# Kernel tuning notes

Measured on AMD Instinct MI355X. Metric: run time of the kernel, lower is better.

## Reference

```python
import jax, jax.numpy as jnp
import numpy as np

N, IN, H, C = 50000, 128, 4, 32
E = 800000
NEG_SLOPE = 0.2


def setup_inputs() -> dict:
    key = jax.random.key(0)
    ks = jax.random.split(key, 8)
    x = jax.random.normal(ks[0], (N, IN), dtype=jnp.float32)
    edge_index = jax.random.randint(ks[1], (2, E), 0, N, dtype=jnp.int64)
    s = 0.1
    W = jax.random.normal(ks[2], (H * C, IN), dtype=jnp.float32) * s
    att_src = jax.random.normal(ks[3], (1, H, C), dtype=jnp.float32) * s
    att_dst = jax.random.normal(ks[4], (1, H, C), dtype=jnp.float32) * s
    bias = jnp.zeros((H * C,), dtype=jnp.float32)
    skip_W = jax.random.normal(ks[5], (H * C, IN), dtype=jnp.float32) * s
    skip_b = jnp.zeros((H * C,), dtype=jnp.float32)
    return {"x": x, "edge_index": edge_index, "W": W, "att_src": att_src,
            "att_dst": att_dst, "bias": bias, "skip_W": skip_W, "skip_b": skip_b}


def reference(x, edge_index, W, att_src, att_dst, bias, skip_W, skip_b):
    src, dst = edge_index[0], edge_index[1]
    # projected node features: [N, H, C]
    xp = (x @ W.T).reshape(N, H, C)
    # per-node attention logits: [N, H]
    a_src = jnp.sum(xp * att_src, axis=-1)
    a_dst = jnp.sum(xp * att_dst, axis=-1)
    # edge logits with LeakyReLU: [E, H]
    e = a_src[src] + a_dst[dst]
    e = jnp.where(e > 0, e, NEG_SLOPE * e)
    # segment softmax over incoming edges of each dst node
    m = jax.ops.segment_max(e, dst, num_segments=N)  # [N, H]
    ex = jnp.exp(e - m[dst])
    denom = jax.ops.segment_sum(ex, dst, num_segments=N)  # [N, H]
    alpha = ex / (denom[dst] + 1e-16)
    # weighted messages and scatter-add aggregation: [N, H, C]
    msg = alpha[:, :, None] * xp[src]
    agg = jax.ops.segment_sum(msg, dst, num_segments=N)
    x_gat = agg.reshape(N, H * C) + bias
    x_skip = x @ skip_W.T + skip_b
    return jax.nn.elu(x_gat + x_skip)
```

## Files before the change

kernel.cpp:

```cpp
#include <hip/hip_runtime.h>
#include <hip/hip_bf16.h>


#define NN 50000
#define EE 800000
#define FD 128
#define NEG_SLOPE 0.2f

#define ROWU 136
#define SCB 1024
#define NB_SC ((NN + SCB - 1) / SCB)
#define NB_PRE 782
#define NB_CONVW 32
#define NB_MFMA (NN / 16)
#define NB_FILL (EE / 256)
#define NB_FUSED (NB_MFMA + NB_FILL)

typedef __attribute__((ext_vector_type(8))) short short8;
typedef __attribute__((ext_vector_type(4))) float f32x4;

__device__ inline ushort f2b(float f) {
    __hip_bfloat16 h = __float2bfloat16(f);
    return *reinterpret_cast<ushort*>(&h);
}
__device__ inline float b2f(ushort u) {
    union { float f; unsigned int i; } c;
    c.i = ((unsigned int)u) << 16;
    return c.f;
}

__global__ __launch_bounds__(256) void gat_pre_kernel(
    const int* __restrict__ idx, int* __restrict__ count, int* __restrict__ rank,
    const float* __restrict__ W, const float* __restrict__ skip_W,
    ushort* __restrict__ wb)
{
    int b = blockIdx.x;
    if (b < NB_PRE) {
        int base = (b * 256 + threadIdx.x) * 4;
        if (base >= EE) return;
        int4 dd = *reinterpret_cast<const int4*>(idx + EE + base);
        int4 rr;
        rr.x = atomicAdd(&count[dd.x], 1);
        rr.y = atomicAdd(&count[dd.y], 1);
        rr.z = atomicAdd(&count[dd.z], 1);
        rr.w = atomicAdd(&count[dd.w], 1);
        *reinterpret_cast<int4*>(rank + base) = rr;
    } else {
        int i = ((b - NB_PRE) * 256 + threadIdx.x) * 4;
        int row = i >> 7;
        int colb = i & 127;
        const float* src = (row < 128) ? (W + row * FD + colb)
                                       : (skip_W + (row - 128) * FD + colb);
        float4 v = *reinterpret_cast<const float4*>(src);
        ushort4 o;
        o.x = f2b(v.x); o.y = f2b(v.y); o.z = f2b(v.z); o.w = f2b(v.w);
        *reinterpret_cast<ushort4*>(wb + i) = o;
    }
}

__global__ __launch_bounds__(1024) void gat_scan_kernel(
    const int* __restrict__ count, int* __restrict__ rowptr)
{
    __shared__ int ws[16];
    __shared__ int boff_s;
    int tid = threadIdx.x, lane = tid & 63, wv = tid >> 6;

    int ps = 0;
    for (int i = tid; i < blockIdx.x * SCB; i += SCB) ps += count[i];
    #pragma unroll
    for (int off = 32; off; off >>= 1) ps += __shfl_down(ps, off, 64);
    if (lane == 0) ws[wv] = ps;
    __syncthreads();
    if (wv == 0) {
        int t = (lane < 16) ? ws[lane] : 0;
        #pragma unroll
        for (int off = 8; off; off >>= 1) t += __shfl_down(t, off, 64);
        if (lane == 0) boff_s = t;
    }
    __syncthreads();

    int i = blockIdx.x * SCB + tid;
    int v = (i < NN) ? count[i] : 0;
    int incl = v;
    #pragma unroll
    for (int off = 1; off < 64; off <<= 1) {
        int t = __shfl_up(incl, off, 64);
        if (lane >= off) incl += t;
    }
    if (lane == 63) ws[wv] = incl;
    __syncthreads();
    if (wv == 0) {
        int t = (lane < 16) ? ws[lane] : 0;
        int winc = t;
        #pragma unroll
        for (int off = 1; off < 16; off <<= 1) {
            int u = __shfl_up(winc, off, 64);
            if (lane >= off) winc += u;
        }
        if (lane < 16) ws[lane] = winc - t;
    }
    __syncthreads();
    int excl = boff_s + ws[wv] + incl - v;
    if (i < NN) rowptr[i] = excl;
    if (blockIdx.x == 0 && tid == 0) rowptr[NN] = EE;
}

__global__ __launch_bounds__(256) void gat_mfma_fill_kernel(
    const float* __restrict__ x, const ushort* __restrict__ wb,
    const float* __restrict__ att_src, const float* __restrict__ att_dst,
    const float* __restrict__ bias, const float* __restrict__ skip_b,
    ushort* __restrict__ xpr, float* __restrict__ a_dst, float* __restrict__ skip,
    const int* __restrict__ idx, const int* __restrict__ rank,
    const int* __restrict__ rowptr, int* __restrict__ col)
{
    const int p = (int)(((long long)blockIdx.x * 2501) % NB_FUSED);
    if (p >= NB_MFMA) {
        int k = (p - NB_MFMA) * 256 + threadIdx.x;
        int d = idx[EE + k];
        int pos = rowptr[d] + rank[k];
        __builtin_nontemporal_store(idx[k], &col[pos]);
        return;
    }

    const int tid = threadIdx.x;
    const int w = tid >> 6;
    const int l = tid & 63;
    const int lrow = l & 15;
    const int lgrp = l >> 4;
    const int m0 = p * 16;
    const int is_skip = w >> 1;
    const int ncb = (w & 1) * 64;

    short8 bfrag[4][4];
    const ushort* wbase = wb + (size_t)(is_skip * 128 + ncb) * FD;
    #pragma unroll
    for (int t = 0; t < 4; ++t)
        #pragma unroll
        for (int kk = 0; kk < 4; ++kk)
            bfrag[t][kk] = *reinterpret_cast<const short8*>(
                wbase + (size_t)(t * 16 + lrow) * FD + kk * 32 + lgrp * 8);

    short8 afrag[4];
    const float* xrow = x + (size_t)(m0 + lrow) * FD + lgrp * 8;
    #pragma unroll
    for (int kk = 0; kk < 4; ++kk) {
        float4 a0 = *reinterpret_cast<const float4*>(xrow + kk * 32);
        float4 a1 = *reinterpret_cast<const float4*>(xrow + kk * 32 + 4);
        short8 af;
        af[0] = f2b(a0.x); af[1] = f2b(a0.y); af[2] = f2b(a0.z); af[3] = f2b(a0.w);
        af[4] = f2b(a1.x); af[5] = f2b(a1.y); af[6] = f2b(a1.z); af[7] = f2b(a1.w);
        afrag[kk] = af;
    }

    f32x4 acc[4];
    #pragma unroll
    for (int t = 0; t < 4; ++t) acc[t] = (f32x4){0.f, 0.f, 0.f, 0.f};

    #pragma unroll
    for (int kk = 0; kk < 4; ++kk)
        #pragma unroll
        for (int t = 0; t < 4; ++t)
            acc[t] = __builtin_amdgcn_mfma_f32_16x16x32_bf16(
                afrag[kk], bfrag[t][kk], acc[t], 0, 0, 0);

    if (is_skip) {
        #pragma unroll
        for (int t = 0; t < 4; ++t) {
            int colt = ncb + t * 16 + lrow;
            float add = skip_b[colt] + bias[colt];
            #pragma unroll
            for (int r = 0; r < 4; ++r) {
                int row = m0 + lgrp * 4 + r;
                skip[(size_t)row * FD + colt] = acc[t][r] + add;
            }
        }
    } else {
        float as[4], ad[4];
        #pragma unroll
        for (int t = 0; t < 4; ++t) {
            int colt = ncb + t * 16 + lrow;
            as[t] = att_src[colt];
            ad[t] = att_dst[colt];
            #pragma unroll
            for (int r = 0; r < 4; ++r) {
                int row = m0 + lgrp * 4 + r;
                xpr[(size_t)row * ROWU + 8 + colt] = f2b(acc[t][r]);
            }
        }
        const int h0 = ncb >> 5;
        #pragma unroll
        for (int r = 0; r < 4; ++r) {
            float p0 = acc[0][r] * as[0] + acc[1][r] * as[1];
            float p1 = acc[2][r] * as[2] + acc[3][r] * as[3];
            float q0 = acc[0][r] * ad[0] + acc[1][r] * ad[1];
            float q1 = acc[2][r] * ad[2] + acc[3][r] * ad[3];
            #pragma unroll
            for (int m = 1; m < 16; m <<= 1) {
                p0 += __shfl_xor(p0, m, 64);
                p1 += __shfl_xor(p1, m, 64);
                q0 += __shfl_xor(q0, m, 64);
                q1 += __shfl_xor(q1, m, 64);
            }
            if (lrow == 0) {
                int row = m0 + lgrp * 4 + r;
                float* arow = reinterpret_cast<float*>(xpr + (size_t)row * ROWU);
                arow[h0]     = p0;
                arow[h0 + 1] = p1;
                a_dst[(size_t)row * 4 + h0]     = q0;
                a_dst[(size_t)row * 4 + h0 + 1] = q1;
            }
        }
    }
}

__global__ __launch_bounds__(256) void gat_gather_kernel(
    const int* __restrict__ rowptr, const int* __restrict__ col,
    const float* __restrict__ a_dst, const ushort* __restrict__ xpr,
    const float* __restrict__ skip, float* __restrict__ out)
{
    int wid = (blockIdx.x * 256 + threadIdx.x) >> 6;
    const int d = __builtin_amdgcn_readfirstlane(wid);
    int lane = threadIdx.x & 63;
    const int h = lane >> 4;
    const int ch = lane * 2;
    const float ad = a_dst[(size_t)d * 4 + h];
    const int beg = rowptr[d], end = rowptr[d + 1];
    float2 sk = *reinterpret_cast<const float2*>(skip + (size_t)d * FD + ch);

    float accx = 0.f, accy = 0.f, asum = 0.f;
    int j = beg;
    for (; j + 8 <= end; j += 8) {
        int s[8];
        float e[8];
        ushort2 xv[8];
        #pragma unroll
        for (int i = 0; i < 8; ++i) s[i] = col[j + i];
        #pragma unroll
        for (int i = 0; i < 8; ++i) {
            const ushort* row = xpr + (size_t)s[i] * ROWU;
            e[i] = reinterpret_cast<const float*>(row)[h] + ad;
            xv[i] = *reinterpret_cast<const ushort2*>(row + 8 + ch);
        }
        #pragma unroll
        for (int i = 0; i < 8; ++i) {
            float ei = e[i];
            ei = ei > 0.f ? ei : NEG_SLOPE * ei;
            float pi = __expf(ei);
            asum += pi;
            accx += pi * b2f(xv[i].x);
            accy += pi * b2f(xv[i].y);
        }
    }
    for (; j < end; ++j) {
        int s = col[j];
        const ushort* row = xpr + (size_t)s * ROWU;
        float e = reinterpret_cast<const float*>(row)[h] + ad;
        ushort2 xv = *reinterpret_cast<const ushort2*>(row + 8 + ch);
        e = e > 0.f ? e : NEG_SLOPE * e;
        float pe = __expf(e);
        asum += pe;
        accx += pe * b2f(xv.x);
        accy += pe * b2f(xv.y);
    }
    float inv = 1.f / (asum + 1e-16f);
    float r0 = sk.x + accx * inv;
    float r1 = sk.y + accy * inv;
    r0 = r0 > 0.f ? r0 : expm1f(r0);
    r1 = r1 > 0.f ? r1 : expm1f(r1);
    *reinterpret_cast<float2*>(out + (size_t)d * FD + ch) = make_float2(r0, r1);
}

extern "C" void kernel_launch(void* const* d_in, const int* in_sizes, int n_in,
                              void* d_out, int out_size, void* d_ws, size_t ws_size,
                              hipStream_t stream)
{
    const float* x       = (const float*)d_in[0];
    const int*   idx     = (const int*)d_in[1];
    const float* W       = (const float*)d_in[2];
    const float* att_src = (const float*)d_in[3];
    const float* att_dst = (const float*)d_in[4];
    const float* bias    = (const float*)d_in[5];
    const float* skip_W  = (const float*)d_in[6];
    const float* skip_b  = (const float*)d_in[7];
    float*       out     = (float*)d_out;

    float*  ws     = (float*)d_ws;
    float*  skip   = ws;
    float*  a_dst  = ws + 6400000;
    int*    count  = (int*)(ws + 6600000);
    int*    rowptr = (int*)(ws + 6652000);
    int*    col    = (int*)(ws + 6756000);
    int*    rank   = (int*)(ws + 7556000);
    ushort* xpr    = (ushort*)(ws + 8400000);
    ushort* wb     = (ushort*)(ws + 11900000);

    hipMemsetAsync(count, 0, (size_t)NN * sizeof(int), stream);

    gat_pre_kernel<<<NB_PRE + NB_CONVW, 256, 0, stream>>>(idx, count, rank, W, skip_W, wb);

    gat_scan_kernel<<<NB_SC, SCB, 0, stream>>>(count, rowptr);

    gat_mfma_fill_kernel<<<NB_FUSED, 256, 0, stream>>>(
        x, wb, att_src, att_dst, bias, skip_b, xpr, a_dst, skip,
        idx, rank, rowptr, col);

    gat_gather_kernel<<<(NN * 64) / 256, 256, 0, stream>>>(
        rowptr, col, a_dst, xpr, skip, out);
}
```

Before: 147.7 us.

## Split a_src from projected rows, class-partition CSR fill, wave-cooperative col loads

The packed xpr row (a_src logits stored inline with the bf16 features) is replaced by a plain bf16 feature array and a separate a_src array. The CSR fill no longer interleaves blocks with the MFMA blocks. It now runs first as 8 destination classes, each class scanning all edges and writing only the edges whose destination falls in its range. The aim is better locality of the scattered col writes. The gather now loads 64 column indices per wave in one go, spreads them with shuffles, and processes 16 edges per step with predicated accumulation. The costs are that every fill block reads the edge list 8 times, and the gather issues wasted loads on the padded tail of each step.

```diff
diff --git a/kernel.cpp b/kernel.cpp
--- a/kernel.cpp
+++ b/kernel.cpp
@@ -7,14 +7,16 @@
 #define FD 128
 #define NEG_SLOPE 0.2f
 
-#define ROWU 136
 #define SCB 1024
 #define NB_SC ((NN + SCB - 1) / SCB)
 #define NB_PRE 782
 #define NB_CONVW 32
+#define NCLS 8
+#define DPC (NN / NCLS)
+#define EPB 2048
+#define QPC ((EE + EPB - 1) / EPB)
+#define NB_FILLB (NCLS * QPC)
 #define NB_MFMA (NN / 16)
-#define NB_FILL (EE / 256)
-#define NB_FUSED (NB_MFMA + NB_FILL)
 
 typedef __attribute__((ext_vector_type(8))) short short8;
 typedef __attribute__((ext_vector_type(4))) float f32x4;
@@ -105,23 +107,33 @@
     if (blockIdx.x == 0 && tid == 0) rowptr[NN] = EE;
 }
 
-__global__ __launch_bounds__(256) void gat_mfma_fill_kernel(
+__global__ __launch_bounds__(256) void gat_fill_mfma_kernel(
     const float* __restrict__ x, const ushort* __restrict__ wb,
     const float* __restrict__ att_src, const float* __restrict__ att_dst,
     const float* __restrict__ bias, const float* __restrict__ skip_b,
-    ushort* __restrict__ xpr, float* __restrict__ a_dst, float* __restrict__ skip,
+    ushort* __restrict__ xpb, float* __restrict__ a_src, float* __restrict__ a_dst,
+    float* __restrict__ skip,
     const int* __restrict__ idx, const int* __restrict__ rank,
     const int* __restrict__ rowptr, int* __restrict__ col)
 {
-    const int p = (int)(((long long)blockIdx.x * 2501) % NB_FUSED);
-    if (p >= NB_MFMA) {
-        int k = (p - NB_MFMA) * 256 + threadIdx.x;
-        int d = idx[EE + k];
-        int pos = rowptr[d] + rank[k];
-        __builtin_nontemporal_store(idx[k], &col[pos]);
+    if (blockIdx.x < NB_FILLB) {
+        const int c = blockIdx.x & (NCLS - 1);
+        const int q = blockIdx.x >> 3;
+        const int dlo = c * DPC, dhi = dlo + DPC;
+        const int k0 = q * EPB + threadIdx.x;
+        #pragma unroll
+        for (int i = 0; i < EPB / 256; ++i) {
+            int k = k0 + i * 256;
+            if (k < EE) {
+                int d = idx[EE + k];
+                if (d >= dlo && d < dhi)
+                    col[rowptr[d] + rank[k]] = idx[k];
+            }
+        }
         return;
     }
 
+    const int p = blockIdx.x - NB_FILLB;
     const int tid = threadIdx.x;
     const int w = tid >> 6;
     const int l = tid & 63;
@@ -184,7 +196,7 @@
             #pragma unroll
             for (int r = 0; r < 4; ++r) {
                 int row = m0 + lgrp * 4 + r;
-                xpr[(size_t)row * ROWU + 8 + colt] = f2b(acc[t][r]);
+                xpb[(size_t)row * FD + colt] = f2b(acc[t][r]);
             }
         }
         const int h0 = ncb >> 5;
@@ -203,9 +215,8 @@
             }
             if (lrow == 0) {
                 int row = m0 + lgrp * 4 + r;
-                float* arow = reinterpret_cast<float*>(xpr + (size_t)row * ROWU);
-                arow[h0]     = p0;
-                arow[h0 + 1] = p1;
+                a_src[(size_t)row * 4 + h0]     = p0;
+                a_src[(size_t)row * 4 + h0 + 1] = p1;
                 a_dst[(size_t)row * 4 + h0]     = q0;
                 a_dst[(size_t)row * 4 + h0 + 1] = q1;
             }
@@ -215,8 +226,9 @@
 
 __global__ __launch_bounds__(256) void gat_gather_kernel(
     const int* __restrict__ rowptr, const int* __restrict__ col,
-    const float* __restrict__ a_dst, const ushort* __restrict__ xpr,
-    const float* __restrict__ skip, float* __restrict__ out)
+    const float* __restrict__ a_src, const float* __restrict__ a_dst,
+    const ushort* __restrict__ xpb, const float* __restrict__ skip,
+    float* __restrict__ out)
 {
     int wid = (blockIdx.x * 256 + threadIdx.x) >> 6;
     const int d = __builtin_amdgcn_readfirstlane(wid);
@@ -228,39 +240,31 @@
     float2 sk = *reinterpret_cast<const float2*>(skip + (size_t)d * FD + ch);
 
     float accx = 0.f, accy = 0.f, asum = 0.f;
-    int j = beg;
-    for (; j + 8 <= end; j += 8) {
-        int s[8];
-        float e[8];
-        ushort2 xv[8];
-        #pragma unroll
-        for (int i = 0; i < 8; ++i) s[i] = col[j + i];
-        #pragma unroll
-        for (int i = 0; i < 8; ++i) {
-            const ushort* row = xpr + (size_t)s[i] * ROWU;
-            e[i] = reinterpret_cast<const float*>(row)[h] + ad;
-            xv[i] = *reinterpret_cast<const ushort2*>(row + 8 + ch);
-        }
-        #pragma unroll
-        for (int i = 0; i < 8; ++i) {
-            float ei = e[i];
+    int sv = 0;
+    for (int base = beg; base < end; base += 16) {
+        int off = (base - beg) & 63;
+        if (off == 0)
+            sv = (base + lane < end) ? col[base + lane] : col[beg];
+        int nb = end - base;
+        float e[16];
+        ushort2 xv[16];
+        #pragma unroll
+        for (int i = 0; i < 16; ++i) {
+            int s = __shfl(sv, off + i, 64);
+            e[i] = a_src[(size_t)s * 4 + h];
+            xv[i] = *reinterpret_cast<const ushort2*>(xpb + (size_t)s * FD + ch);
+        }
+        #pragma unroll
+        for (int i = 0; i < 16; ++i) {
+            float ei = e[i] + ad;
             ei = ei > 0.f ? ei : NEG_SLOPE * ei;
             float pi = __expf(ei);
-            asum += pi;
-            accx += pi * b2f(xv[i].x);
-            accy += pi * b2f(xv[i].y);
-        }
-    }
-    for (; j < end; ++j) {
-        int s = col[j];
-        const ushort* row = xpr + (size_t)s * ROWU;
-        float e = reinterpret_cast<const float*>(row)[h] + ad;
-        ushort2 xv = *reinterpret_cast<const ushort2*>(row + 8 + ch);
-        e = e > 0.f ? e : NEG_SLOPE * e;
-        float pe = __expf(e);
-        asum += pe;
-        accx += pe * b2f(xv.x);
-        accy += pe * b2f(xv.y);
+            if (i < nb) {
+                asum += pi;
+                accx += pi * b2f(xv[i].x);
+                accy += pi * b2f(xv[i].y);
+            }
+        }
     }
     float inv = 1.f / (asum + 1e-16f);
     float r0 = sk.x + accx * inv;
@@ -286,12 +290,13 @@
 
     float*  ws     = (float*)d_ws;
     float*  skip   = ws;
-    float*  a_dst  = ws + 6400000;
-    int*    count  = (int*)(ws + 6600000);
-    int*    rowptr = (int*)(ws + 6652000);
-    int*    col    = (int*)(ws + 6756000);
-    int*    rank   = (int*)(ws + 7556000);
-    ushort* xpr    = (ushort*)(ws + 8400000);
+    float*  a_src  = ws + 6400000;
+    float*  a_dst  = ws + 6600000;
+    int*    count  = (int*)(ws + 6800000);
+    int*    rowptr = (int*)(ws + 6852000);
+    int*    col    = (int*)(ws + 6956000);
+    int*    rank   = (int*)(ws + 7756000);
+    ushort* xpb    = (ushort*)(ws + 8600000);
     ushort* wb     = (ushort*)(ws + 11900000);
 
     hipMemsetAsync(count, 0, (size_t)NN * sizeof(int), stream);
@@ -300,10 +305,10 @@
 
     gat_scan_kernel<<<NB_SC, SCB, 0, stream>>>(count, rowptr);
 
-    gat_mfma_fill_kernel<<<NB_FUSED, 256, 0, stream>>>(
-        x, wb, att_src, att_dst, bias, skip_b, xpr, a_dst, skip,
+    gat_fill_mfma_kernel<<<NB_FILLB + NB_MFMA, 256, 0, stream>>>(
+        x, wb, att_src, att_dst, bias, skip_b, xpb, a_src, a_dst, skip,
         idx, rank, rowptr, col);
 
     gat_gather_kernel<<<(NN * 64) / 256, 256, 0, stream>>>(
-        rowptr, col, a_dst, xpr, skip, out);
-}
+        rowptr, col, a_src, a_dst, xpb, skip, out);
+}
```

After: 149.6 us. Within noise of the previous version (+1.3%).
